# Kernel optimization log

Hardware: AMD Instinct MI355X
Metric: run time of the kernel (lower is better)

The kernel has to match this reference:

```python
import jax, jax.numpy as jnp
import numpy as np

B, S = 1, 2048
HS = 2048          # hidden_size
H, KV, D = 16, 8, 128   # num_heads, num_kv_heads, head_dim
IM = 6144          # intermediate_size
EPS = 1e-6
BASE = 10000.0


def rmsnorm(x, w, eps=EPS):
    v = jnp.mean(jnp.square(x.astype(jnp.float32)), axis=-1, keepdims=True)
    return (x.astype(jnp.float32) * jax.lax.rsqrt(v + eps)).astype(x.dtype) * w


def apply_rope(x, pos):
    # x: [B,S,nh,D], pos: [B,S]
    half = x.shape[-1] // 2
    inv_freq = 1.0 / (BASE ** (jnp.arange(half, dtype=jnp.float32) / half))
    ang = pos.astype(jnp.float32)[..., None] * inv_freq            # [B,S,half]
    cos = jnp.concatenate([jnp.cos(ang)] * 2, -1)[:, :, None, :]   # [B,S,1,D]
    sin = jnp.concatenate([jnp.sin(ang)] * 2, -1)[:, :, None, :]
    x1, x2 = jnp.split(x, 2, axis=-1)
    rot = jnp.concatenate([-x2, x1], axis=-1)                      # rotate_half
    return x * cos + rot * sin


def setup_inputs() -> dict:
    key = jax.random.key(0)
    ks = jax.random.split(key, 13)
    s = 0.02
    return {
        "x": jax.random.normal(ks[0], (B, S, HS), jnp.float32),
        "position_ids": jnp.broadcast_to(jnp.arange(S, dtype=jnp.int64), (B, S)),
        "w_in_norm": jnp.ones((HS,), jnp.float32),
        "wq": jax.random.normal(ks[1], (HS, H * D), jnp.float32) * s,
        "wk": jax.random.normal(ks[2], (HS, KV * D), jnp.float32) * s,
        "wv": jax.random.normal(ks[3], (HS, KV * D), jnp.float32) * s,
        "q_norm_w": jnp.ones((D,), jnp.float32),
        "k_norm_w": jnp.ones((D,), jnp.float32),
        "wo": jax.random.normal(ks[4], (H * D, HS), jnp.float32) * s,
        "w_post_norm": jnp.ones((HS,), jnp.float32),
        "w_gate": jax.random.normal(ks[5], (HS, IM), jnp.float32) * s,
        "w_up": jax.random.normal(ks[6], (HS, IM), jnp.float32) * s,
        "w_down": jax.random.normal(ks[7], (IM, HS), jnp.float32) * s,
    }


def reference(x, position_ids, w_in_norm, wq, wk, wv, q_norm_w, k_norm_w, wo,
              w_post_norm, w_gate, w_up, w_down):
    # --- attention sub-block ---
    h = rmsnorm(x, w_in_norm)
    q = (h @ wq).reshape(B, S, H, D)
    k = (h @ wk).reshape(B, S, KV, D)
    v = (h @ wv).reshape(B, S, KV, D)
    # per-head QK RMSNorm (Qwen3 qk_norm)
    q = rmsnorm(q, q_norm_w)
    k = rmsnorm(k, k_norm_w)
    q = apply_rope(q, position_ids)
    k = apply_rope(k, position_ids)
    # GQA: repeat kv heads to match query heads
    rep = H // KV
    k = jnp.repeat(k, rep, axis=2)   # [B,S,H,D]
    v = jnp.repeat(v, rep, axis=2)
    scores = jnp.einsum('bqhd,bkhd->bhqk', q, k) * (D ** -0.5)
    causal = jnp.tril(jnp.ones((S, S), bool))
    scores = jnp.where(causal, scores, jnp.finfo(scores.dtype).min)
    p = jax.nn.softmax(scores, axis=-1)
    attn = jnp.einsum('bhqk,bkhd->bqhd', p, v).reshape(B, S, H * D)
    x = x + attn @ wo
    # --- MLP sub-block (SwiGLU) ---
    h = rmsnorm(x, w_post_norm)
    mlp = (jax.nn.silu(h @ w_gate) * (h @ w_up)) @ w_down
    return x + mlp
```

## Files before the change

### kernel.cpp

```cpp
#include <hip/hip_runtime.h>
#include <math.h>

#define SEQ   2048
#define HSZ   2048
#define NHQ   16
#define NKV   8
#define HD    128
#define IMS   6144
#define EPSF  1e-6f

typedef float f32x4 __attribute__((ext_vector_type(4)));
typedef short s16x8 __attribute__((ext_vector_type(8)));

__device__ __forceinline__ unsigned short f2bf(float f) {
    unsigned int u = __float_as_uint(f);
    unsigned int r = (u + 0x7FFFu + ((u >> 16) & 1u)) >> 16;
    return (unsigned short)r;
}
__device__ __forceinline__ float bf2f(unsigned short h) {
    return __uint_as_float(((unsigned int)h) << 16);
}

__global__ __launch_bounds__(256) void rmsnorm_kernel(
    const float* __restrict__ x, const float* __restrict__ w,
    float* __restrict__ out, int ncols)
{
    const int row = blockIdx.x;
    const float* xr = x + (size_t)row * ncols;
    float* orow = out + (size_t)row * ncols;
    float ssq = 0.f;
    for (int c = threadIdx.x * 4; c < ncols; c += 256 * 4) {
        float4 v = *reinterpret_cast<const float4*>(xr + c);
        ssq += v.x*v.x + v.y*v.y + v.z*v.z + v.w*v.w;
    }
#pragma unroll
    for (int off = 32; off; off >>= 1) ssq += __shfl_down(ssq, off, 64);
    __shared__ float red[4];
    __shared__ float rs_s;
    if ((threadIdx.x & 63) == 0) red[threadIdx.x >> 6] = ssq;
    __syncthreads();
    if (threadIdx.x == 0) {
        float t = red[0] + red[1] + red[2] + red[3];
        rs_s = rsqrtf(t / (float)ncols + EPSF);
    }
    __syncthreads();
    const float rs = rs_s;
    for (int c = threadIdx.x * 4; c < ncols; c += 256 * 4) {
        float4 v = *reinterpret_cast<const float4*>(xr + c);
        float4 g = *reinterpret_cast<const float4*>(w + c);
        float4 o;
        o.x = v.x * rs * g.x; o.y = v.y * rs * g.y;
        o.z = v.z * rs * g.z; o.w = v.w * rs * g.w;
        *reinterpret_cast<float4*>(orow + c) = o;
    }
}

__global__ __launch_bounds__(256) void rmsnorm_planes_kernel(
    const float* __restrict__ x, const float* __restrict__ w,
    unsigned short* __restrict__ Ph, unsigned short* __restrict__ Pl,
    int ncols, int M)
{
    const int row = blockIdx.x;
    const float* xr = x + (size_t)row * ncols;
    const int c0 = threadIdx.x * 8;
    float4 v0 = *reinterpret_cast<const float4*>(xr + c0);
    float4 v1 = *reinterpret_cast<const float4*>(xr + c0 + 4);
    float ssq = v0.x*v0.x + v0.y*v0.y + v0.z*v0.z + v0.w*v0.w
              + v1.x*v1.x + v1.y*v1.y + v1.z*v1.z + v1.w*v1.w;
#pragma unroll
    for (int off = 32; off; off >>= 1) ssq += __shfl_down(ssq, off, 64);
    __shared__ float red[4];
    __shared__ float rs_s;
    if ((threadIdx.x & 63) == 0) red[threadIdx.x >> 6] = ssq;
    __syncthreads();
    if (threadIdx.x == 0)
        rs_s = rsqrtf((red[0] + red[1] + red[2] + red[3]) / (float)ncols + EPSF);
    __syncthreads();
    const float rs = rs_s;
    float vals[8] = {v0.x, v0.y, v0.z, v0.w, v1.x, v1.y, v1.z, v1.w};
    unsigned short hh[8], ll[8];
#pragma unroll
    for (int i = 0; i < 8; ++i) {
        float f = vals[i] * rs * w[c0 + i];
        hh[i] = f2bf(f);
        ll[i] = f2bf(f - bf2f(hh[i]));
    }
    const size_t boff = ((size_t)threadIdx.x * M + row) * 8;
    uint4 ph, pl;
    ph.x = hh[0] | (hh[1] << 16); ph.y = hh[2] | (hh[3] << 16);
    ph.z = hh[4] | (hh[5] << 16); ph.w = hh[6] | (hh[7] << 16);
    pl.x = ll[0] | (ll[1] << 16); pl.y = ll[2] | (ll[3] << 16);
    pl.z = ll[4] | (ll[5] << 16); pl.w = ll[6] | (ll[7] << 16);
    *reinterpret_cast<uint4*>(Ph + boff) = ph;
    *reinterpret_cast<uint4*>(Pl + boff) = pl;
}

__global__ __launch_bounds__(256) void wconv_kernel(
    const float* __restrict__ W, unsigned short* __restrict__ Ph,
    unsigned short* __restrict__ Pl, int Kd, int Nd)
{
    const int idx = blockIdx.x * 256 + threadIdx.x;
    const int total = (Kd >> 3) * Nd;
    if (idx >= total) return;
    const int kb = idx / Nd;
    const int n  = idx - kb * Nd;
    unsigned short hh[8], ll[8];
#pragma unroll
    for (int i = 0; i < 8; ++i) {
        float f = W[(size_t)(kb * 8 + i) * Nd + n];
        hh[i] = f2bf(f);
        ll[i] = f2bf(f - bf2f(hh[i]));
    }
    uint4 ph, pl;
    ph.x = hh[0] | (hh[1] << 16); ph.y = hh[2] | (hh[3] << 16);
    ph.z = hh[4] | (hh[5] << 16); ph.w = hh[6] | (hh[7] << 16);
    pl.x = ll[0] | (ll[1] << 16); pl.y = ll[2] | (ll[3] << 16);
    pl.z = ll[4] | (ll[5] << 16); pl.w = ll[6] | (ll[7] << 16);
    *reinterpret_cast<uint4*>(Ph + (size_t)idx * 8) = ph;
    *reinterpret_cast<uint4*>(Pl + (size_t)idx * 8) = pl;
}

__global__ __launch_bounds__(256) void sgemm128(
    const float* __restrict__ A, const float* __restrict__ B,
    const float* __restrict__ R, float* __restrict__ C,
    int M, int N, int K)
{
    __shared__ float As[16][128];
    __shared__ float Bs[16][128];
    const int tid = threadIdx.x;
    const int tx = tid & 15;
    const int ty = tid >> 4;
    const int bm = blockIdx.y, bn = blockIdx.x;
    const int arow = tid >> 2;
    const int acol = (tid & 3) << 2;
    const int brow = tid >> 5;
    const int bcol = (tid & 31) << 2;
    const float* Ap = A + (size_t)(bm * 128 + arow) * K + acol;
    const float* Bp = B + (size_t)brow * N + bn * 128 + bcol;
    float acc[8][8] = {};

    float4 a0 = *reinterpret_cast<const float4*>(Ap);
    float4 a1 = *reinterpret_cast<const float4*>(Ap + (size_t)64 * K);
    float4 b0 = *reinterpret_cast<const float4*>(Bp);
    float4 b1 = *reinterpret_cast<const float4*>(Bp + (size_t)8 * N);

    for (int k0 = 0;;) {
        __syncthreads();
        As[acol + 0][arow] = a0.x; As[acol + 1][arow] = a0.y;
        As[acol + 2][arow] = a0.z; As[acol + 3][arow] = a0.w;
        As[acol + 0][arow + 64] = a1.x; As[acol + 1][arow + 64] = a1.y;
        As[acol + 2][arow + 64] = a1.z; As[acol + 3][arow + 64] = a1.w;
        *reinterpret_cast<float4*>(&Bs[brow][bcol]) = b0;
        *reinterpret_cast<float4*>(&Bs[brow + 8][bcol]) = b1;
        __syncthreads();
        const int kn = k0 + 16;
        float4 na0, na1, nb0, nb1;
        if (kn < K) {
            na0 = *reinterpret_cast<const float4*>(Ap + kn);
            na1 = *reinterpret_cast<const float4*>(Ap + (size_t)64 * K + kn);
            nb0 = *reinterpret_cast<const float4*>(Bp + (size_t)kn * N);
            nb1 = *reinterpret_cast<const float4*>(Bp + (size_t)(kn + 8) * N);
        }
#pragma unroll
        for (int kk = 0; kk < 16; ++kk) {
            float4 av0 = *reinterpret_cast<const float4*>(&As[kk][ty * 8]);
            float4 av1 = *reinterpret_cast<const float4*>(&As[kk][ty * 8 + 4]);
            float4 bv0 = *reinterpret_cast<const float4*>(&Bs[kk][tx * 8]);
            float4 bv1 = *reinterpret_cast<const float4*>(&Bs[kk][tx * 8 + 4]);
            float a[8] = {av0.x, av0.y, av0.z, av0.w, av1.x, av1.y, av1.z, av1.w};
            float b[8] = {bv0.x, bv0.y, bv0.z, bv0.w, bv1.x, bv1.y, bv1.z, bv1.w};
#pragma unroll
            for (int i = 0; i < 8; ++i)
#pragma unroll
                for (int j = 0; j < 8; ++j)
                    acc[i][j] += a[i] * b[j];
        }
        if (kn >= K) break;
        a0 = na0; a1 = na1; b0 = nb0; b1 = nb1;
        k0 = kn;
    }

    const int row0 = bm * 128 + ty * 8;
    const int col0 = bn * 128 + tx * 8;
#pragma unroll
    for (int i = 0; i < 8; ++i) {
        size_t off = (size_t)(row0 + i) * N + col0;
        float4 o0 = make_float4(acc[i][0], acc[i][1], acc[i][2], acc[i][3]);
        float4 o1 = make_float4(acc[i][4], acc[i][5], acc[i][6], acc[i][7]);
        if (R) {
            float4 r0 = *reinterpret_cast<const float4*>(R + off);
            float4 r1 = *reinterpret_cast<const float4*>(R + off + 4);
            o0.x += r0.x; o0.y += r0.y; o0.z += r0.z; o0.w += r0.w;
            o1.x += r1.x; o1.y += r1.y; o1.z += r1.z; o1.w += r1.w;
        }
        *reinterpret_cast<float4*>(C + off) = o0;
        *reinterpret_cast<float4*>(C + off + 4) = o1;
    }
}

template<int EPI>
__global__ __launch_bounds__(256) void mgemm3(
    const unsigned short* __restrict__ Ah, const unsigned short* __restrict__ Al,
    const unsigned short* __restrict__ Bh, const unsigned short* __restrict__ Bl,
    const float* __restrict__ X, float* __restrict__ C,
    unsigned short* __restrict__ Oh, unsigned short* __restrict__ Ol,
    int M, int N, int K)
{
    __shared__ uint4 Sl[4][512];

    const int tid  = threadIdx.x;
    const int lane = tid & 63;
    const int wid  = tid >> 6;
    const int wm   = wid >> 1, wn = wid & 1;
    const int bm = blockIdx.y, bn = blockIdx.x;

    const uint4* gplane;
    {
        const unsigned short* p = (wid == 0) ? Ah : (wid == 1) ? Al : (wid == 2) ? Bh : Bl;
        gplane = reinterpret_cast<const uint4*>(p);
    }
    const int pdim  = (wid < 2) ? M : N;
    const int pbase = (wid < 2) ? bm * 128 : bn * 128;

    f32x4 acc[4][4];
#pragma unroll
    for (int i = 0; i < 4; ++i)
#pragma unroll
        for (int j = 0; j < 4; ++j)
            acc[i][j] = (f32x4){0.f, 0.f, 0.f, 0.f};

    const int steps = K >> 5;
    uint4 rg[8];
#pragma unroll
    for (int i = 0; i < 8; ++i) {
        const int kb = i >> 1, idx = (i & 1) * 64 + lane;
        rg[i] = gplane[(size_t)kb * pdim + pbase + idx];
    }

    for (int s = 0; s < steps; ++s) {
        __syncthreads();
#pragma unroll
        for (int i = 0; i < 8; ++i) {
            const int kb = i >> 1, idx = (i & 1) * 64 + lane;
            Sl[wid][kb * 128 + idx] = rg[i];
        }
        __syncthreads();
        if (s + 1 < steps) {
            const size_t kb0 = (size_t)(s + 1) * 4;
#pragma unroll
            for (int i = 0; i < 8; ++i) {
                const int kb = i >> 1, idx = (i & 1) * 64 + lane;
                rg[i] = gplane[(kb0 + kb) * pdim + pbase + idx];
            }
        }
        const int kq = (lane >> 4) * 128 + (lane & 15);
        s16x8 bh[4], bl[4];
#pragma unroll
        for (int nf = 0; nf < 4; ++nf) {
            bh[nf] = *reinterpret_cast<const s16x8*>(&Sl[2][kq + wn * 64 + nf * 16]);
            bl[nf] = *reinterpret_cast<const s16x8*>(&Sl[3][kq + wn * 64 + nf * 16]);
        }
#pragma unroll
        for (int mf = 0; mf < 4; ++mf) {
            s16x8 ah = *reinterpret_cast<const s16x8*>(&Sl[0][kq + wm * 64 + mf * 16]);
            s16x8 al = *reinterpret_cast<const s16x8*>(&Sl[1][kq + wm * 64 + mf * 16]);
#pragma unroll
            for (int nf = 0; nf < 4; ++nf) {
                acc[mf][nf] = __builtin_amdgcn_mfma_f32_16x16x32_bf16(ah, bh[nf], acc[mf][nf], 0, 0, 0);
                acc[mf][nf] = __builtin_amdgcn_mfma_f32_16x16x32_bf16(al, bh[nf], acc[mf][nf], 0, 0, 0);
                acc[mf][nf] = __builtin_amdgcn_mfma_f32_16x16x32_bf16(ah, bl[nf], acc[mf][nf], 0, 0, 0);
            }
        }
    }

    const int lrow = (lane >> 4) * 4;
    const int lcol = lane & 15;
#pragma unroll
    for (int mf = 0; mf < 4; ++mf) {
#pragma unroll
        for (int nf = 0; nf < 4; ++nf) {
            const int col = bn * 128 + wn * 64 + nf * 16 + lcol;
            const int row0 = bm * 128 + wm * 64 + mf * 16 + lrow;
#pragma unroll
            for (int r = 0; r < 4; ++r) {
                const int row = row0 + r;
                float val = acc[mf][nf][r];
                if (EPI == 0) {
                    if (X) val += X[(size_t)row * N + col];
                    C[(size_t)row * N + col] = val;
                } else {
                    const float g = X[(size_t)row * N + col];
                    const float sg = g / (1.f + expf(-g));
                    const float v = sg * val;
                    const unsigned short h = f2bf(v);
                    const unsigned short l = f2bf(v - bf2f(h));
                    const size_t po = ((size_t)(col >> 3) * M + row) * 8 + (col & 7);
                    Oh[po] = h;
                    Ol[po] = l;
                }
            }
        }
    }
}

__global__ __launch_bounds__(128) void qknorm_rope_kernel(
    float* __restrict__ x, const float* __restrict__ w,
    const int* __restrict__ pos, int nheads)
{
    const int blk = blockIdx.x;
    const int s = blk / nheads, hh = blk - s * nheads;
    float* xr = x + ((size_t)s * nheads + hh) * HD;
    const int d = threadIdx.x;
    float vv = xr[d];
    float ssq = vv * vv;
#pragma unroll
    for (int off = 32; off; off >>= 1) ssq += __shfl_down(ssq, off, 64);
    __shared__ float red2[2];
    __shared__ float xn[HD];
    if ((d & 63) == 0) red2[d >> 6] = ssq;
    __syncthreads();
    const float rs = rsqrtf((red2[0] + red2[1]) * (1.f / HD) + EPSF);
    const float nv = vv * rs * w[d];
    xn[d] = nv;
    __syncthreads();
    const float p = (float)pos[s];
    const int i = d & 63;
    const float inv_freq = expf(-0.14391156698f * (float)i);
    const float ang = p * inv_freq;
    float sn, cs;
    sincosf(ang, &sn, &cs);
    const float rot = (d < 64) ? -xn[d + 64] : xn[d - 64];
    xr[d] = nv * cs + rot * sn;
}

__global__ __launch_bounds__(256) void attn3_kernel(
    const float* __restrict__ Q, const float* __restrict__ K,
    const float* __restrict__ V, float* __restrict__ O)
{
    __shared__ float Qt[128 * 64];
    __shared__ float KT[128 * 64];

    const int h = blockIdx.y;
    const int bx = blockIdx.x;
    const int qt_idx = (bx & 1) ? (31 - (bx >> 1)) : (bx >> 1);
    const int q0 = qt_idx * 64;
    const int kvh = h >> 1;
    const int tid = threadIdx.x;
    const int tr = tid >> 4, tc = tid & 15;
    const int lane = tid & 63;
    const int gbase = lane & 48;
    const int nt = (q0 >> 6) + 1;
    const float scale = 0.08838834764831845f;

    {
        const int qr = tid & 63;
        const int dbase = (tid >> 6) * 4;
        const float* qp = Q + (size_t)(q0 + qr) * (NHQ * HD) + h * HD;
#pragma unroll
        for (int it = 0; it < 8; ++it) {
            const int d0 = dbase + it * 16;
            float4 qv = *reinterpret_cast<const float4*>(qp + d0);
            Qt[(d0 + 0) * 64 + qr] = qv.x * scale;
            Qt[(d0 + 1) * 64 + qr] = qv.y * scale;
            Qt[(d0 + 2) * 64 + qr] = qv.z * scale;
            Qt[(d0 + 3) * 64 + qr] = qv.w * scale;
        }
    }

    const int kj = tid & 63;
    const int kd = (tid >> 6) * 4;
    const float* kbp = K + (size_t)kvh * HD + kd;
    float4 kreg[8];
#pragma unroll
    for (int it = 0; it < 8; ++it)
        kreg[it] = *reinterpret_cast<const float4*>(kbp + (size_t)kj * (NKV * HD) + it * 16);

    float sc[4][4], p[4][4];
    float4 oA[4], oB[4];
    float mrow[4], lrow[4];
#pragma unroll
    for (int i = 0; i < 4; ++i) {
        oA[i] = make_float4(0.f, 0.f, 0.f, 0.f);
        oB[i] = make_float4(0.f, 0.f, 0.f, 0.f);
        mrow[i] = -INFINITY; lrow[i] = 0.f;
    }

    for (int t = 0; t < nt; ++t) {
        const int j0 = t * 64;
        __syncthreads();
#pragma unroll
        for (int it = 0; it < 8; ++it) {
            const int d0 = kd + it * 16;
            KT[(d0 + 0) * 64 + kj] = kreg[it].x;
            KT[(d0 + 1) * 64 + kj] = kreg[it].y;
            KT[(d0 + 2) * 64 + kj] = kreg[it].z;
            KT[(d0 + 3) * 64 + kj] = kreg[it].w;
        }
        __syncthreads();
        if (t + 1 < nt) {
#pragma unroll
            for (int it = 0; it < 8; ++it)
                kreg[it] = *reinterpret_cast<const float4*>(
                    kbp + (size_t)((t + 1) * 64 + kj) * (NKV * HD) + it * 16);
        }

#pragma unroll
        for (int i = 0; i < 4; ++i)
#pragma unroll
            for (int c = 0; c < 4; ++c) sc[i][c] = 0.f;
#pragma unroll 4
        for (int kk = 0; kk < 128; ++kk) {
            float4 qv = *reinterpret_cast<const float4*>(&Qt[kk * 64 + tr * 4]);
            float4 kv = *reinterpret_cast<const float4*>(&KT[kk * 64 + tc * 4]);
            float qa[4] = {qv.x, qv.y, qv.z, qv.w};
            float ka[4] = {kv.x, kv.y, kv.z, kv.w};
#pragma unroll
            for (int i = 0; i < 4; ++i)
#pragma unroll
                for (int c = 0; c < 4; ++c)
                    sc[i][c] += qa[i] * ka[c];
        }

        if (j0 == q0) {
#pragma unroll
            for (int i = 0; i < 4; ++i) {
                const int r = tr * 4 + i;
#pragma unroll
                for (int c = 0; c < 4; ++c)
                    if (tc * 4 + c > r) sc[i][c] = -INFINITY;
            }
        }

#pragma unroll
        for (int i = 0; i < 4; ++i) {
            float rm = fmaxf(fmaxf(sc[i][0], sc[i][1]), fmaxf(sc[i][2], sc[i][3]));
            rm = fmaxf(rm, __shfl_xor(rm, 1, 64));
            rm = fmaxf(rm, __shfl_xor(rm, 2, 64));
            rm = fmaxf(rm, __shfl_xor(rm, 4, 64));
            rm = fmaxf(rm, __shfl_xor(rm, 8, 64));
            const float mnew = fmaxf(mrow[i], rm);
            const float fac = expf(mrow[i] - mnew);
            mrow[i] = mnew;
            float rsum = 0.f;
#pragma unroll
            for (int c = 0; c < 4; ++c) {
                const float e = expf(sc[i][c] - mnew);
                p[i][c] = e; rsum += e;
            }
            rsum += __shfl_xor(rsum, 1, 64);
            rsum += __shfl_xor(rsum, 2, 64);
            rsum += __shfl_xor(rsum, 4, 64);
            rsum += __shfl_xor(rsum, 8, 64);
            lrow[i] = lrow[i] * fac + rsum;
            oA[i].x *= fac; oA[i].y *= fac; oA[i].z *= fac; oA[i].w *= fac;
            oB[i].x *= fac; oB[i].y *= fac; oB[i].z *= fac; oB[i].w *= fac;
        }

        const float* vb = V + (size_t)j0 * (NKV * HD) + kvh * HD + tc * 8;
#pragma unroll
        for (int j4 = 0; j4 < 16; ++j4) {
            float pb[4][4];
#pragma unroll
            for (int i = 0; i < 4; ++i)
#pragma unroll
                for (int c = 0; c < 4; ++c)
                    pb[i][c] = __shfl(p[i][c], gbase + j4, 64);
#pragma unroll
            for (int c = 0; c < 4; ++c) {
                const int j = j4 * 4 + c;
                const float* vr = vb + (size_t)j * (NKV * HD);
                float4 v0 = *reinterpret_cast<const float4*>(vr);
                float4 v1 = *reinterpret_cast<const float4*>(vr + 4);
#pragma unroll
                for (int i = 0; i < 4; ++i) {
                    oA[i].x += pb[i][c] * v0.x; oA[i].y += pb[i][c] * v0.y;
                    oA[i].z += pb[i][c] * v0.z; oA[i].w += pb[i][c] * v0.w;
                    oB[i].x += pb[i][c] * v1.x; oB[i].y += pb[i][c] * v1.y;
                    oB[i].z += pb[i][c] * v1.z; oB[i].w += pb[i][c] * v1.w;
                }
            }
        }
    }

#pragma unroll
    for (int i = 0; i < 4; ++i) {
        const float inv = 1.f / lrow[i];
        float4 a = oA[i], b = oB[i];
        a.x *= inv; a.y *= inv; a.z *= inv; a.w *= inv;
        b.x *= inv; b.y *= inv; b.z *= inv; b.w *= inv;
        const size_t off = (size_t)(q0 + tr * 4 + i) * (NHQ * HD) + h * HD + tc * 8;
        *reinterpret_cast<float4*>(O + off) = a;
        *reinterpret_cast<float4*>(O + off + 4) = b;
    }
}

extern "C" void kernel_launch(void* const* d_in, const int* in_sizes, int n_in,
                              void* d_out, int out_size, void* d_ws, size_t ws_size,
                              hipStream_t stream)
{
    const float* x     = (const float*)d_in[0];
    const int*   pos   = (const int*)d_in[1];
    const float* w_in  = (const float*)d_in[2];
    const float* wq    = (const float*)d_in[3];
    const float* wk    = (const float*)d_in[4];
    const float* wv    = (const float*)d_in[5];
    const float* qnw   = (const float*)d_in[6];
    const float* knw   = (const float*)d_in[7];
    const float* wo    = (const float*)d_in[8];
    const float* wpost = (const float*)d_in[9];
    const float* wgate = (const float*)d_in[10];
    const float* wup   = (const float*)d_in[11];
    const float* wdown = (const float*)d_in[12];
    float* out = (float*)d_out;

    float* ws   = (float*)d_ws;
    float* h    = ws;
    float* q    = h + (size_t)SEQ * HSZ;
    float* k    = q + (size_t)SEQ * NHQ * HD;
    float* v    = k + (size_t)SEQ * NKV * HD;
    float* gate = v + (size_t)SEQ * NKV * HD;
    unsigned short* gah = (unsigned short*)(gate + (size_t)SEQ * IMS);
    unsigned short* gal = gah + (size_t)SEQ * IMS;
    unsigned short* wbh = gal + (size_t)SEQ * IMS;
    unsigned short* wbl = wbh + (size_t)HSZ * IMS;
    unsigned short* h2h = (unsigned short*)q;
    unsigned short* h2l = h2h + (size_t)SEQ * HSZ;

    rmsnorm_kernel<<<SEQ, 256, 0, stream>>>(x, w_in, h, HSZ);
    sgemm128<<<dim3((NHQ * HD) / 128, SEQ / 128), 256, 0, stream>>>(h, wq, nullptr, q, SEQ, NHQ * HD, HSZ);
    sgemm128<<<dim3((NKV * HD) / 128, SEQ / 128), 256, 0, stream>>>(h, wk, nullptr, k, SEQ, NKV * HD, HSZ);
    sgemm128<<<dim3((NKV * HD) / 128, SEQ / 128), 256, 0, stream>>>(h, wv, nullptr, v, SEQ, NKV * HD, HSZ);
    qknorm_rope_kernel<<<SEQ * NHQ, 128, 0, stream>>>(q, qnw, pos, NHQ);
    qknorm_rope_kernel<<<SEQ * NKV, 128, 0, stream>>>(k, knw, pos, NKV);
    attn3_kernel<<<dim3(SEQ / 64, NHQ), 256, 0, stream>>>(q, k, v, h);
    sgemm128<<<dim3(HSZ / 128, SEQ / 128), 256, 0, stream>>>(h, wo, x, out, SEQ, HSZ, NHQ * HD);

    rmsnorm_planes_kernel<<<SEQ, 256, 0, stream>>>(out, wpost, h2h, h2l, HSZ, SEQ);
    wconv_kernel<<<(HSZ / 8) * IMS / 256, 256, 0, stream>>>(wgate, wbh, wbl, HSZ, IMS);
    mgemm3<0><<<dim3(IMS / 128, SEQ / 128), 256, 0, stream>>>(
        h2h, h2l, wbh, wbl, nullptr, gate, nullptr, nullptr, SEQ, IMS, HSZ);
    wconv_kernel<<<(HSZ / 8) * IMS / 256, 256, 0, stream>>>(wup, wbh, wbl, HSZ, IMS);
    mgemm3<1><<<dim3(IMS / 128, SEQ / 128), 256, 0, stream>>>(
        h2h, h2l, wbh, wbl, gate, nullptr, gah, gal, SEQ, IMS, HSZ);
    wconv_kernel<<<(IMS / 8) * HSZ / 256, 256, 0, stream>>>(wdown, wbh, wbl, IMS, HSZ);
    mgemm3<0><<<dim3(HSZ / 128, SEQ / 128), 256, 0, stream>>>(
        gah, gal, wbh, wbl, out, out, nullptr, nullptr, SEQ, HSZ, IMS);
}
```

Measured before the change: 3.246 ms.

## Move attention and O-projection to bf16 MFMA with split-precision operands

Replaces the scalar FP32 flash-attention kernel with an MFMA bf16 version. Q is split into hi/lo bf16 planes, K and V are single bf16 packed layouts, and P is written through LDS. The O-projection moves from the FP32 SGEMM to the split-bf16 MFMA GEMM, with attention output emitted directly as hi/lo planes. New conversion kernels for V and wo are added. This cuts FP32 ALU work but lowers precision for K, V and P and adds extra conversion passes.

```diff
diff --git a/kernel.cpp b/kernel.cpp
--- a/kernel.cpp
+++ b/kernel.cpp
@@ -303,13 +303,14 @@
     }
 }
 
-__global__ __launch_bounds__(128) void qknorm_rope_kernel(
-    float* __restrict__ x, const float* __restrict__ w,
-    const int* __restrict__ pos, int nheads)
+__global__ __launch_bounds__(128) void qknorm_rope2_kernel(
+    const float* __restrict__ x, const float* __restrict__ w,
+    const int* __restrict__ pos, unsigned short* __restrict__ Ph,
+    unsigned short* __restrict__ Pl, int nheads, float scale)
 {
     const int blk = blockIdx.x;
     const int s = blk / nheads, hh = blk - s * nheads;
-    float* xr = x + ((size_t)s * nheads + hh) * HD;
+    const float* xr = x + ((size_t)s * nheads + hh) * HD;
     const int d = threadIdx.x;
     float vv = xr[d];
     float ssq = vv * vv;
@@ -330,167 +331,193 @@
     float sn, cs;
     sincosf(ang, &sn, &cs);
     const float rot = (d < 64) ? -xn[d + 64] : xn[d - 64];
-    xr[d] = nv * cs + rot * sn;
-}
-
-__global__ __launch_bounds__(256) void attn3_kernel(
-    const float* __restrict__ Q, const float* __restrict__ K,
-    const float* __restrict__ V, float* __restrict__ O)
-{
-    __shared__ float Qt[128 * 64];
-    __shared__ float KT[128 * 64];
+    const float val = (nv * cs + rot * sn) * scale;
+    const unsigned short hi = f2bf(val);
+    const size_t idx = ((size_t)(hh * 16 + (d >> 3)) * 2048 + s) * 8 + (d & 7);
+    Ph[idx] = hi;
+    if (Pl) Pl[idx] = f2bf(val - bf2f(hi));
+}
+
+__global__ __launch_bounds__(256) void vconv_kernel(
+    const float* __restrict__ v, unsigned short* __restrict__ Vp)
+{
+    const int kvh = blockIdx.y;
+    const int k0 = blockIdx.x * 64;
+    const int d = threadIdx.x & 127;
+    const int half = threadIdx.x >> 7;
+    uint4* Vp4 = reinterpret_cast<uint4*>(Vp) + (size_t)kvh * 256 * 128;
+#pragma unroll
+    for (int kb = half * 4; kb < half * 4 + 4; ++kb) {
+        unsigned short t8[8];
+#pragma unroll
+        for (int j = 0; j < 8; ++j)
+            t8[j] = f2bf(v[(size_t)(k0 + kb * 8 + j) * (NKV * HD) + kvh * HD + d]);
+        uint4 u;
+        u.x = (unsigned)t8[0] | ((unsigned)t8[1] << 16);
+        u.y = (unsigned)t8[2] | ((unsigned)t8[3] << 16);
+        u.z = (unsigned)t8[4] | ((unsigned)t8[5] << 16);
+        u.w = (unsigned)t8[6] | ((unsigned)t8[7] << 16);
+        Vp4[(size_t)((k0 >> 3) + kb) * 128 + d] = u;
+    }
+}
+
+__global__ __launch_bounds__(256) void attn4_kernel(
+    const unsigned short* __restrict__ Qh, const unsigned short* __restrict__ Ql,
+    const unsigned short* __restrict__ Kh, const unsigned short* __restrict__ Vh,
+    unsigned short* __restrict__ Oh, unsigned short* __restrict__ Ol)
+{
+    __shared__ uint4 sK[16 * 65];
+    __shared__ uint4 sV[8 * 129];
+    __shared__ __align__(16) unsigned short sP[4][32 * 72];
 
     const int h = blockIdx.y;
-    const int bx = blockIdx.x;
-    const int qt_idx = (bx & 1) ? (31 - (bx >> 1)) : (bx >> 1);
-    const int q0 = qt_idx * 64;
     const int kvh = h >> 1;
+    const int qb0 = blockIdx.x * 128;
     const int tid = threadIdx.x;
-    const int tr = tid >> 4, tc = tid & 15;
     const int lane = tid & 63;
-    const int gbase = lane & 48;
-    const int nt = (q0 >> 6) + 1;
-    const float scale = 0.08838834764831845f;
-
-    {
-        const int qr = tid & 63;
-        const int dbase = (tid >> 6) * 4;
-        const float* qp = Q + (size_t)(q0 + qr) * (NHQ * HD) + h * HD;
-#pragma unroll
-        for (int it = 0; it < 8; ++it) {
-            const int d0 = dbase + it * 16;
-            float4 qv = *reinterpret_cast<const float4*>(qp + d0);
-            Qt[(d0 + 0) * 64 + qr] = qv.x * scale;
-            Qt[(d0 + 1) * 64 + qr] = qv.y * scale;
-            Qt[(d0 + 2) * 64 + qr] = qv.z * scale;
-            Qt[(d0 + 3) * 64 + qr] = qv.w * scale;
-        }
-    }
-
-    const int kj = tid & 63;
-    const int kd = (tid >> 6) * 4;
-    const float* kbp = K + (size_t)kvh * HD + kd;
-    float4 kreg[8];
-#pragma unroll
-    for (int it = 0; it < 8; ++it)
-        kreg[it] = *reinterpret_cast<const float4*>(kbp + (size_t)kj * (NKV * HD) + it * 16);
-
-    float sc[4][4], p[4][4];
-    float4 oA[4], oB[4];
-    float mrow[4], lrow[4];
-#pragma unroll
-    for (int i = 0; i < 4; ++i) {
-        oA[i] = make_float4(0.f, 0.f, 0.f, 0.f);
-        oB[i] = make_float4(0.f, 0.f, 0.f, 0.f);
-        mrow[i] = -INFINITY; lrow[i] = 0.f;
-    }
-
+    const int w = tid >> 6;
+    const int g = lane >> 4;
+    const int l15 = lane & 15;
+    const int qw0 = qb0 + w * 32;
+
+    const uint4* Qh4 = reinterpret_cast<const uint4*>(Qh) + (size_t)h * 16 * 2048;
+    const uint4* Ql4 = reinterpret_cast<const uint4*>(Ql) + (size_t)h * 16 * 2048;
+    s16x8 qfh[2][4], qfl[2][4];
+#pragma unroll
+    for (int mf = 0; mf < 2; ++mf)
+#pragma unroll
+        for (int kb = 0; kb < 4; ++kb) {
+            const int idx = (kb * 4 + g) * 2048 + qw0 + mf * 16 + l15;
+            uint4 a = Qh4[idx], b = Ql4[idx];
+            qfh[mf][kb] = *reinterpret_cast<s16x8*>(&a);
+            qfl[mf][kb] = *reinterpret_cast<s16x8*>(&b);
+        }
+
+    f32x4 o[2][8];
+    float m[2][4], lsum[2][4];
+#pragma unroll
+    for (int mf = 0; mf < 2; ++mf) {
+#pragma unroll
+        for (int f = 0; f < 8; ++f) o[mf][f] = (f32x4){0.f, 0.f, 0.f, 0.f};
+#pragma unroll
+        for (int r = 0; r < 4; ++r) { m[mf][r] = -INFINITY; lsum[mf][r] = 0.f; }
+    }
+
+    const uint4* Kg0 = reinterpret_cast<const uint4*>(Kh) + (size_t)kvh * 16 * 2048;
+    const uint4* Vg0 = reinterpret_cast<const uint4*>(Vh) + (size_t)kvh * 256 * 128;
+
+    const int nt = qb0 / 64 + 2;
     for (int t = 0; t < nt; ++t) {
         const int j0 = t * 64;
         __syncthreads();
-#pragma unroll
-        for (int it = 0; it < 8; ++it) {
-            const int d0 = kd + it * 16;
-            KT[(d0 + 0) * 64 + kj] = kreg[it].x;
-            KT[(d0 + 1) * 64 + kj] = kreg[it].y;
-            KT[(d0 + 2) * 64 + kj] = kreg[it].z;
-            KT[(d0 + 3) * 64 + kj] = kreg[it].w;
+        {
+            const int dblk = tid >> 4, kk = tid & 15;
+            const uint4* Kg = Kg0 + j0;
+#pragma unroll
+            for (int s = 0; s < 4; ++s)
+                sK[dblk * 65 + kk + s * 16] = Kg[(size_t)dblk * 2048 + kk + s * 16];
+            const int kl = tid >> 5, dd = tid & 31;
+            const uint4* Vg = Vg0 + (size_t)(j0 >> 3) * 128;
+#pragma unroll
+            for (int s = 0; s < 4; ++s)
+                sV[kl * 129 + dd + s * 32] = Vg[(size_t)kl * 128 + dd + s * 32];
         }
         __syncthreads();
-        if (t + 1 < nt) {
-#pragma unroll
-            for (int it = 0; it < 8; ++it)
-                kreg[it] = *reinterpret_cast<const float4*>(
-                    kbp + (size_t)((t + 1) * 64 + kj) * (NKV * HD) + it * 16);
-        }
-
-#pragma unroll
-        for (int i = 0; i < 4; ++i)
-#pragma unroll
-            for (int c = 0; c < 4; ++c) sc[i][c] = 0.f;
-#pragma unroll 4
-        for (int kk = 0; kk < 128; ++kk) {
-            float4 qv = *reinterpret_cast<const float4*>(&Qt[kk * 64 + tr * 4]);
-            float4 kv = *reinterpret_cast<const float4*>(&KT[kk * 64 + tc * 4]);
-            float qa[4] = {qv.x, qv.y, qv.z, qv.w};
-            float ka[4] = {kv.x, kv.y, kv.z, kv.w};
-#pragma unroll
-            for (int i = 0; i < 4; ++i)
-#pragma unroll
-                for (int c = 0; c < 4; ++c)
-                    sc[i][c] += qa[i] * ka[c];
-        }
-
-        if (j0 == q0) {
-#pragma unroll
-            for (int i = 0; i < 4; ++i) {
-                const int r = tr * 4 + i;
-#pragma unroll
-                for (int c = 0; c < 4; ++c)
-                    if (tc * 4 + c > r) sc[i][c] = -INFINITY;
-            }
-        }
-
-#pragma unroll
-        for (int i = 0; i < 4; ++i) {
-            float rm = fmaxf(fmaxf(sc[i][0], sc[i][1]), fmaxf(sc[i][2], sc[i][3]));
-            rm = fmaxf(rm, __shfl_xor(rm, 1, 64));
-            rm = fmaxf(rm, __shfl_xor(rm, 2, 64));
-            rm = fmaxf(rm, __shfl_xor(rm, 4, 64));
-            rm = fmaxf(rm, __shfl_xor(rm, 8, 64));
-            const float mnew = fmaxf(mrow[i], rm);
-            const float fac = expf(mrow[i] - mnew);
-            mrow[i] = mnew;
-            float rsum = 0.f;
-#pragma unroll
-            for (int c = 0; c < 4; ++c) {
-                const float e = expf(sc[i][c] - mnew);
-                p[i][c] = e; rsum += e;
-            }
-            rsum += __shfl_xor(rsum, 1, 64);
-            rsum += __shfl_xor(rsum, 2, 64);
-            rsum += __shfl_xor(rsum, 4, 64);
-            rsum += __shfl_xor(rsum, 8, 64);
-            lrow[i] = lrow[i] * fac + rsum;
-            oA[i].x *= fac; oA[i].y *= fac; oA[i].z *= fac; oA[i].w *= fac;
-            oB[i].x *= fac; oB[i].y *= fac; oB[i].z *= fac; oB[i].w *= fac;
-        }
-
-        const float* vb = V + (size_t)j0 * (NKV * HD) + kvh * HD + tc * 8;
-#pragma unroll
-        for (int j4 = 0; j4 < 16; ++j4) {
-            float pb[4][4];
-#pragma unroll
-            for (int i = 0; i < 4; ++i)
-#pragma unroll
-                for (int c = 0; c < 4; ++c)
-                    pb[i][c] = __shfl(p[i][c], gbase + j4, 64);
-#pragma unroll
-            for (int c = 0; c < 4; ++c) {
-                const int j = j4 * 4 + c;
-                const float* vr = vb + (size_t)j * (NKV * HD);
-                float4 v0 = *reinterpret_cast<const float4*>(vr);
-                float4 v1 = *reinterpret_cast<const float4*>(vr + 4);
-#pragma unroll
-                for (int i = 0; i < 4; ++i) {
-                    oA[i].x += pb[i][c] * v0.x; oA[i].y += pb[i][c] * v0.y;
-                    oA[i].z += pb[i][c] * v0.z; oA[i].w += pb[i][c] * v0.w;
-                    oB[i].x += pb[i][c] * v1.x; oB[i].y += pb[i][c] * v1.y;
-                    oB[i].z += pb[i][c] * v1.z; oB[i].w += pb[i][c] * v1.w;
+        if (j0 > qw0 + 31) continue;
+
+        f32x4 sc[2][4];
+#pragma unroll
+        for (int mf = 0; mf < 2; ++mf)
+#pragma unroll
+            for (int fc = 0; fc < 4; ++fc) sc[mf][fc] = (f32x4){0.f, 0.f, 0.f, 0.f};
+#pragma unroll
+        for (int kb = 0; kb < 4; ++kb)
+#pragma unroll
+            for (int fc = 0; fc < 4; ++fc) {
+                uint4 kr = sK[(kb * 4 + g) * 65 + fc * 16 + l15];
+                s16x8 kf = *reinterpret_cast<s16x8*>(&kr);
+#pragma unroll
+                for (int mf = 0; mf < 2; ++mf) {
+                    sc[mf][fc] = __builtin_amdgcn_mfma_f32_16x16x32_bf16(qfh[mf][kb], kf, sc[mf][fc], 0, 0, 0);
+                    sc[mf][fc] = __builtin_amdgcn_mfma_f32_16x16x32_bf16(qfl[mf][kb], kf, sc[mf][fc], 0, 0, 0);
                 }
             }
-        }
-    }
-
-#pragma unroll
-    for (int i = 0; i < 4; ++i) {
-        const float inv = 1.f / lrow[i];
-        float4 a = oA[i], b = oB[i];
-        a.x *= inv; a.y *= inv; a.z *= inv; a.w *= inv;
-        b.x *= inv; b.y *= inv; b.z *= inv; b.w *= inv;
-        const size_t off = (size_t)(q0 + tr * 4 + i) * (NHQ * HD) + h * HD + tc * 8;
-        *reinterpret_cast<float4*>(O + off) = a;
-        *reinterpret_cast<float4*>(O + off + 4) = b;
+
+        const bool mk = (j0 + 63 > qw0);
+#pragma unroll
+        for (int mf = 0; mf < 2; ++mf)
+#pragma unroll
+            for (int r = 0; r < 4; ++r) {
+                float sv0 = sc[mf][0][r], sv1 = sc[mf][1][r];
+                float sv2 = sc[mf][2][r], sv3 = sc[mf][3][r];
+                if (mk) {
+                    const int q = qw0 + mf * 16 + g * 4 + r;
+                    if (j0 +  0 + l15 > q) sv0 = -INFINITY;
+                    if (j0 + 16 + l15 > q) sv1 = -INFINITY;
+                    if (j0 + 32 + l15 > q) sv2 = -INFINITY;
+                    if (j0 + 48 + l15 > q) sv3 = -INFINITY;
+                }
+                float rm = fmaxf(fmaxf(sv0, sv1), fmaxf(sv2, sv3));
+                rm = fmaxf(rm, __shfl_xor(rm, 1, 64));
+                rm = fmaxf(rm, __shfl_xor(rm, 2, 64));
+                rm = fmaxf(rm, __shfl_xor(rm, 4, 64));
+                rm = fmaxf(rm, __shfl_xor(rm, 8, 64));
+                const float mn = fmaxf(m[mf][r], rm);
+                const float fac = __expf(m[mf][r] - mn);
+                m[mf][r] = mn;
+                const float p0 = __expf(sv0 - mn), p1 = __expf(sv1 - mn);
+                const float p2 = __expf(sv2 - mn), p3 = __expf(sv3 - mn);
+                float rs = p0 + p1 + p2 + p3;
+                rs += __shfl_xor(rs, 1, 64);
+                rs += __shfl_xor(rs, 2, 64);
+                rs += __shfl_xor(rs, 4, 64);
+                rs += __shfl_xor(rs, 8, 64);
+                lsum[mf][r] = lsum[mf][r] * fac + rs;
+#pragma unroll
+                for (int f = 0; f < 8; ++f) o[mf][f][r] *= fac;
+                unsigned short* pw = &sP[w][(mf * 16 + g * 4 + r) * 72];
+                pw[ 0 + l15] = f2bf(p0);
+                pw[16 + l15] = f2bf(p1);
+                pw[32 + l15] = f2bf(p2);
+                pw[48 + l15] = f2bf(p3);
+            }
+
+#pragma unroll
+        for (int ks = 0; ks < 2; ++ks) {
+            s16x8 pa[2];
+#pragma unroll
+            for (int mf = 0; mf < 2; ++mf)
+                pa[mf] = *reinterpret_cast<const s16x8*>(
+                    &sP[w][(mf * 16 + l15) * 72 + ks * 32 + g * 8]);
+#pragma unroll
+            for (int f = 0; f < 8; ++f) {
+                uint4 vr = sV[(ks * 4 + g) * 129 + f * 16 + l15];
+                s16x8 vf = *reinterpret_cast<s16x8*>(&vr);
+#pragma unroll
+                for (int mf = 0; mf < 2; ++mf)
+                    o[mf][f] = __builtin_amdgcn_mfma_f32_16x16x32_bf16(pa[mf], vf, o[mf][f], 0, 0, 0);
+            }
+        }
+    }
+
+#pragma unroll
+    for (int mf = 0; mf < 2; ++mf) {
+        float inv[4];
+#pragma unroll
+        for (int r = 0; r < 4; ++r) inv[r] = 1.f / lsum[mf][r];
+#pragma unroll
+        for (int f = 0; f < 8; ++f) {
+            const int col = h * 128 + f * 16 + l15;
+#pragma unroll
+            for (int r = 0; r < 4; ++r) {
+                const int row = qb0 + w * 32 + mf * 16 + g * 4 + r;
+                const float val = o[mf][f][r] * inv[r];
+                const size_t idx = ((size_t)(col >> 3) * 2048 + row) * 8 + (col & 7);
+                const unsigned short hi = f2bf(val);
+                Oh[idx] = hi;
+                Ol[idx] = f2bf(val - bf2f(hi));
+            }
+        }
     }
 }
 
@@ -513,27 +540,37 @@
     const float* wdown = (const float*)d_in[12];
     float* out = (float*)d_out;
 
-    float* ws   = (float*)d_ws;
+    const size_t M1 = 1024 * 1024;
+    float* ws = (float*)d_ws;
     float* h    = ws;
-    float* q    = h + (size_t)SEQ * HSZ;
-    float* k    = q + (size_t)SEQ * NHQ * HD;
-    float* v    = k + (size_t)SEQ * NKV * HD;
-    float* gate = v + (size_t)SEQ * NKV * HD;
-    unsigned short* gah = (unsigned short*)(gate + (size_t)SEQ * IMS);
-    unsigned short* gal = gah + (size_t)SEQ * IMS;
-    unsigned short* wbh = gal + (size_t)SEQ * IMS;
-    unsigned short* wbl = wbh + (size_t)HSZ * IMS;
-    unsigned short* h2h = (unsigned short*)q;
-    unsigned short* h2l = h2h + (size_t)SEQ * HSZ;
+    float* qf   = ws + 4 * M1;
+    float* kf   = ws + 8 * M1;
+    float* vf   = ws + 10 * M1;
+    float* gate = ws + 12 * M1;
+    unsigned short* QhP = (unsigned short*)(ws + 12 * M1);
+    unsigned short* QlP = QhP + 4 * M1;
+    unsigned short* KhP = QlP + 4 * M1;
+    unsigned short* VhP = KhP + 2 * M1;
+    unsigned short* gah = (unsigned short*)(ws + 24 * M1);
+    unsigned short* gal = gah + 12 * M1;
+    unsigned short* OhP = (unsigned short*)(ws + 24 * M1);
+    unsigned short* OlP = OhP + 4 * M1;
+    unsigned short* wbh = (unsigned short*)(ws + 36 * M1);
+    unsigned short* wbl = wbh + 12 * M1;
+    unsigned short* h2h = (unsigned short*)qf;
+    unsigned short* h2l = h2h + 4 * M1;
 
     rmsnorm_kernel<<<SEQ, 256, 0, stream>>>(x, w_in, h, HSZ);
-    sgemm128<<<dim3((NHQ * HD) / 128, SEQ / 128), 256, 0, stream>>>(h, wq, nullptr, q, SEQ, NHQ * HD, HSZ);
-    sgemm128<<<dim3((NKV * HD) / 128, SEQ / 128), 256, 0, stream>>>(h, wk, nullptr, k, SEQ, NKV * HD, HSZ);
-    sgemm128<<<dim3((NKV * HD) / 128, SEQ / 128), 256, 0, stream>>>(h, wv, nullptr, v, SEQ, NKV * HD, HSZ);
-    qknorm_rope_kernel<<<SEQ * NHQ, 128, 0, stream>>>(q, qnw, pos, NHQ);
-    qknorm_rope_kernel<<<SEQ * NKV, 128, 0, stream>>>(k, knw, pos, NKV);
-    attn3_kernel<<<dim3(SEQ / 64, NHQ), 256, 0, stream>>>(q, k, v, h);
-    sgemm128<<<dim3(HSZ / 128, SEQ / 128), 256, 0, stream>>>(h, wo, x, out, SEQ, HSZ, NHQ * HD);
+    sgemm128<<<dim3((NHQ * HD) / 128, SEQ / 128), 256, 0, stream>>>(h, wq, nullptr, qf, SEQ, NHQ * HD, HSZ);
+    sgemm128<<<dim3((NKV * HD) / 128, SEQ / 128), 256, 0, stream>>>(h, wk, nullptr, kf, SEQ, NKV * HD, HSZ);
+    sgemm128<<<dim3((NKV * HD) / 128, SEQ / 128), 256, 0, stream>>>(h, wv, nullptr, vf, SEQ, NKV * HD, HSZ);
+    qknorm_rope2_kernel<<<SEQ * NHQ, 128, 0, stream>>>(qf, qnw, pos, QhP, QlP, NHQ, 0.08838834764831845f);
+    qknorm_rope2_kernel<<<SEQ * NKV, 128, 0, stream>>>(kf, knw, pos, KhP, nullptr, NKV, 1.0f);
+    vconv_kernel<<<dim3(32, NKV), 256, 0, stream>>>(vf, VhP);
+    attn4_kernel<<<dim3(SEQ / 128, NHQ), 256, 0, stream>>>(QhP, QlP, KhP, VhP, OhP, OlP);
+    wconv_kernel<<<(HSZ / 8) * HSZ / 256, 256, 0, stream>>>(wo, wbh, wbl, HSZ, HSZ);
+    mgemm3<0><<<dim3(HSZ / 128, SEQ / 128), 256, 0, stream>>>(
+        OhP, OlP, wbh, wbl, x, out, nullptr, nullptr, SEQ, HSZ, HSZ);
 
     rmsnorm_planes_kernel<<<SEQ, 256, 0, stream>>>(out, wpost, h2h, h2l, HSZ, SEQ);
     wconv_kernel<<<(HSZ / 8) * IMS / 256, 256, 0, stream>>>(wgate, wbh, wbl, HSZ, IMS);
```

After: 2.665 ms. 17.9% less time.
